# Kernel tuning notes

Hardware: AMD Instinct MI355X
Metric: run time of the kernel (lower is better)

Reference implementation:

```python
import jax, jax.numpy as jnp
import numpy as np

BIAS = 7  # FP8 E4M3 exponent bias


def _decode(bits):
    # bits [..., 8] in order [s, e3, e2, e1, e0, m2, m1, m0]
    b = bits.astype(jnp.int32)
    s = b[..., 0]
    e = (b[..., 1] << 3) | (b[..., 2] << 2) | (b[..., 3] << 1) | b[..., 4]
    m = (b[..., 5] << 2) | (b[..., 6] << 1) | b[..., 7]
    return s, e, m


def _rne_rshift(M, sh):
    # round-to-nearest-even right shift of non-negative int M by sh (sh >= 0)
    q = M >> sh
    rem = M - (q << sh)
    half = jnp.right_shift(jnp.left_shift(1, sh), 1)  # 2^(sh-1), 0 when sh==0
    up = ((rem > half) | ((rem == half) & ((q & 1) == 1))) & (sh > 0)
    return q + up.astype(jnp.int32)


def setup_inputs() -> dict:
    key = jax.random.key(0)
    ks = jax.random.split(key, 6)
    shape = (1024, 4096)

    def make(k1, k2, k3):
        s = jax.random.randint(k1, shape, 0, 2)
        e = jax.random.randint(k2, shape, 0, 15)  # exclude e=15 (NaN region) for well-defined inputs
        m = jax.random.randint(k3, shape, 0, 8)
        bits = jnp.stack([s, (e >> 3) & 1, (e >> 2) & 1, (e >> 1) & 1, e & 1,
                          (m >> 2) & 1, (m >> 1) & 1, m & 1], axis=-1)
        return bits.astype(jnp.float32)

    return {"a": make(ks[0], ks[1], ks[2]), "b": make(ks[3], ks[4], ks[5])}


def _fp8_mul(a, b):
    sa, ea, ma = _decode(a)
    sb, eb_, mb = _decode(b)
    # significand with implicit bit; subnormals (e==0) use leading-zero-normalized form,
    # identical math to the module's mux_a_leading / shift_calc path
    sig_a = jnp.where(ea == 0, ma, ma + 8)
    sig_b = jnp.where(eb_ == 0, mb, mb + 8)
    exa = jnp.where(ea == 0, 1, ea) - BIAS
    exb = jnp.where(eb_ == 0, 1, eb_) - BIAS
    M = sig_a * sig_b              # exact 8-bit product, <= 225 (the 4x4 array multiplier)
    E = exa + exb - 6              # value = M * 2^E  (each sig in units of 2^-3)
    # MSB position p of M (M in [1, 225] => p in [0, 7])
    p = sum(((M >= (1 << k)).astype(jnp.int32) for k in range(1, 8)), start=jnp.zeros_like(M))
    eb_out = E + p + BIAS          # candidate biased exponent (normalization unit)
    # ---- normal path (eb_out >= 1): RNE round to 3 mantissa bits ----
    sh = p - 3
    shp = jnp.maximum(sh, 0)
    lsh = jnp.maximum(-sh, 0)
    mant4 = jnp.left_shift(_rne_rshift(M, shp), lsh)  # in [8, 16]
    carry = mant4 >> 4                                # rounding overflow -> exp += 1
    mant4 = jnp.where(mant4 == 16, 8, mant4)
    e_n = eb_out + carry
    m_n = mant4 - 8
    nan = e_n >= 16                                   # exponent overflow -> NaN (e=1111, m=111)
    e_n = jnp.where(nan, 15, e_n)
    m_n = jnp.where(nan, 7, m_n)
    # ---- subnormal path (eb_out <= 0): mant = RNE(M * 2^(E+9)), value = mant * 2^-9 ----
    t = E + 9
    mant_s = jnp.left_shift(_rne_rshift(M, jnp.clip(-t, 0, 30)), jnp.maximum(t, 0))
    e_s = jnp.where(mant_s >= 8, 1, 0)                # rounding promoted to smallest normal
    m_s = jnp.where(mant_s >= 8, 0, mant_s)
    # ---- select ----
    is_sub = eb_out <= 0
    e_o = jnp.where(is_sub, e_s, e_n)
    m_o = jnp.where(is_sub, m_s, m_n)
    zero = M == 0                                     # either input true zero
    e_o = jnp.where(zero, 0, e_o)
    m_o = jnp.where(zero, 0, m_o)
    s_o = sa ^ sb
    bits = jnp.stack([s_o, (e_o >> 3) & 1, (e_o >> 2) & 1, (e_o >> 1) & 1, e_o & 1,
                      (m_o >> 2) & 1, (m_o >> 1) & 1, m_o & 1], axis=-1)
    return bits.astype(jnp.float32)


def reference(a, b):
    return _fp8_mul(a, b)
```

## Files before the change

kernel.cpp:

```cpp
#include <hip/hip_runtime.h>


#define BIAS 7

__device__ __forceinline__ int rne_rshift(int M, int sh) {
    int q = M >> sh;
    int rem = M - (q << sh);
    int half = (1 << sh) >> 1;
    int up = ((rem > half) | ((rem == half) & (q & 1))) & (sh > 0);
    return q + up;
}

__global__ void __launch_bounds__(256)
fp8_mul_kernel(const float4* __restrict__ a, const float4* __restrict__ b,
               float4* __restrict__ out, int n_groups) {
    int i = blockIdx.x * blockDim.x + threadIdx.x;
    if (i >= n_groups) return;

    float4 a0 = a[2 * i];
    float4 a1 = a[2 * i + 1];
    float4 b0 = b[2 * i];
    float4 b1 = b[2 * i + 1];

    int sa = (int)a0.x;
    int ea = ((int)a0.y << 3) | ((int)a0.z << 2) | ((int)a0.w << 1) | (int)a1.x;
    int ma = ((int)a1.y << 2) | ((int)a1.z << 1) | (int)a1.w;
    int sb = (int)b0.x;
    int eb = ((int)b0.y << 3) | ((int)b0.z << 2) | ((int)b0.w << 1) | (int)b1.x;
    int mb = ((int)b1.y << 2) | ((int)b1.z << 1) | (int)b1.w;

    int sig_a = (ea == 0) ? ma : (ma + 8);
    int sig_b = (eb == 0) ? mb : (mb + 8);
    int exa = ((ea == 0) ? 1 : ea) - BIAS;
    int exb = ((eb == 0) ? 1 : eb) - BIAS;

    int M = sig_a * sig_b;
    int E = exa + exb - 6;

    int p = (M > 0) ? (31 - __clz(M)) : 0;
    int eb_out = E + p + BIAS;

    int sh  = p - 3;
    int shp = (sh > 0) ? sh : 0;
    int lsh = (sh < 0) ? -sh : 0;
    int mant4 = rne_rshift(M, shp) << lsh;
    int carry = mant4 >> 4;
    if (mant4 == 16) mant4 = 8;
    int e_n = eb_out + carry;
    int m_n = mant4 - 8;
    if (e_n >= 16) { e_n = 15; m_n = 7; }

    int t = E + 9;
    int rsh = (-t < 0) ? 0 : ((-t > 30) ? 30 : -t);
    int lsh_s = (t > 0) ? t : 0;
    int mant_s = rne_rshift(M, rsh) << lsh_s;
    int e_s = (mant_s >= 8) ? 1 : 0;
    int m_s = (mant_s >= 8) ? 0 : mant_s;

    int is_sub = (eb_out <= 0);
    int e_o = is_sub ? e_s : e_n;
    int m_o = is_sub ? m_s : m_n;
    if (M == 0) { e_o = 0; m_o = 0; }
    int s_o = sa ^ sb;

    float4 o0, o1;
    o0.x = (float)s_o;
    o0.y = (float)((e_o >> 3) & 1);
    o0.z = (float)((e_o >> 2) & 1);
    o0.w = (float)((e_o >> 1) & 1);
    o1.x = (float)(e_o & 1);
    o1.y = (float)((m_o >> 2) & 1);
    o1.z = (float)((m_o >> 1) & 1);
    o1.w = (float)(m_o & 1);
    out[2 * i]     = o0;
    out[2 * i + 1] = o1;
}

extern "C" void kernel_launch(void* const* d_in, const int* in_sizes, int n_in,
                              void* d_out, int out_size, void* d_ws, size_t ws_size,
                              hipStream_t stream) {
    const float4* a = (const float4*)d_in[0];
    const float4* b = (const float4*)d_in[1];
    float4* out = (float4*)d_out;
    int n_groups = in_sizes[0] / 8;
    int block = 256;
    int grid = (n_groups + block - 1) / block;
    fp8_mul_kernel<<<grid, block, 0, stream>>>(a, b, out, n_groups);
}
```

Measured before the change: 302.6 us.

## Split each FP8 element across two lanes with shuffle exchange and bit-test loads

Each thread now loads one float4 (half of an element's 8 bit-floats) from each input and reads the bits as uint nonzero tests instead of float-to-int conversions. The two lanes of a pair swap nibbles via __shfl_xor, both redundantly compute the FP8 product, and each writes its own half of the output. This doubles thread count and makes every lane access a contiguous 16-byte vector, aiming for better memory coalescing and more loads in flight on a bandwidth-bound kernel. The cost is duplicated arithmetic and a cross-lane shuffle per element.

```diff
diff --git a/kernel.cpp b/kernel.cpp
--- a/kernel.cpp
+++ b/kernel.cpp
@@ -11,23 +11,10 @@
     return q + up;
 }
 
-__global__ void __launch_bounds__(256)
-fp8_mul_kernel(const float4* __restrict__ a, const float4* __restrict__ b,
-               float4* __restrict__ out, int n_groups) {
-    int i = blockIdx.x * blockDim.x + threadIdx.x;
-    if (i >= n_groups) return;
-
-    float4 a0 = a[2 * i];
-    float4 a1 = a[2 * i + 1];
-    float4 b0 = b[2 * i];
-    float4 b1 = b[2 * i + 1];
-
-    int sa = (int)a0.x;
-    int ea = ((int)a0.y << 3) | ((int)a0.z << 2) | ((int)a0.w << 1) | (int)a1.x;
-    int ma = ((int)a1.y << 2) | ((int)a1.z << 1) | (int)a1.w;
-    int sb = (int)b0.x;
-    int eb = ((int)b0.y << 3) | ((int)b0.z << 2) | ((int)b0.w << 1) | (int)b1.x;
-    int mb = ((int)b1.y << 2) | ((int)b1.z << 1) | (int)b1.w;
+__device__ __forceinline__ int fp8_mul_byte(int a8, int b8) {
+    int sa = a8 >> 7,        sb_ = b8 >> 7;
+    int ea = (a8 >> 3) & 15, eb = (b8 >> 3) & 15;
+    int ma = a8 & 7,         mb = b8 & 7;
 
     int sig_a = (ea == 0) ? ma : (ma + 8);
     int sig_b = (eb == 0) ? mb : (mb + 8);
@@ -51,7 +38,7 @@
     if (e_n >= 16) { e_n = 15; m_n = 7; }
 
     int t = E + 9;
-    int rsh = (-t < 0) ? 0 : ((-t > 30) ? 30 : -t);
+    int rsh   = (-t < 0) ? 0 : ((-t > 30) ? 30 : -t);
     int lsh_s = (t > 0) ? t : 0;
     int mant_s = rne_rshift(M, rsh) << lsh_s;
     int e_s = (mant_s >= 8) ? 1 : 0;
@@ -61,29 +48,49 @@
     int e_o = is_sub ? e_s : e_n;
     int m_o = is_sub ? m_s : m_n;
     if (M == 0) { e_o = 0; m_o = 0; }
-    int s_o = sa ^ sb;
+    int s_o = sa ^ sb_;
+    return (s_o << 7) | (e_o << 3) | m_o;
+}
 
-    float4 o0, o1;
-    o0.x = (float)s_o;
-    o0.y = (float)((e_o >> 3) & 1);
-    o0.z = (float)((e_o >> 2) & 1);
-    o0.w = (float)((e_o >> 1) & 1);
-    o1.x = (float)(e_o & 1);
-    o1.y = (float)((m_o >> 2) & 1);
-    o1.z = (float)((m_o >> 1) & 1);
-    o1.w = (float)(m_o & 1);
-    out[2 * i]     = o0;
-    out[2 * i + 1] = o1;
+__global__ void __launch_bounds__(256)
+fp8_mul_kernel(const uint4* __restrict__ a, const uint4* __restrict__ b,
+               float4* __restrict__ out, int n_vec) {
+    int j = blockIdx.x * blockDim.x + threadIdx.x;
+    if (j >= n_vec) return;
+
+    uint4 av = a[j];
+    uint4 bv = b[j];
+
+    int na = ((av.x != 0) << 3) | ((av.y != 0) << 2) | ((av.z != 0) << 1) | (int)(av.w != 0);
+    int nb = ((bv.x != 0) << 3) | ((bv.y != 0) << 2) | ((bv.z != 0) << 1) | (int)(bv.w != 0);
+    int own = na | (nb << 4);
+    int pp  = __shfl_xor(own, 1);
+
+    int odd = j & 1;
+    int a8 = odd ? (((pp  & 0xF) << 4) |  (own & 0xF))
+                 : (((own & 0xF) << 4) |  (pp  & 0xF));
+    int b8 = odd ? ((((pp  >> 4) & 0xF) << 4) | ((own >> 4) & 0xF))
+                 : ((((own >> 4) & 0xF) << 4) | ((pp  >> 4) & 0xF));
+
+    int r = fp8_mul_byte(a8, b8);
+
+    int sbit = odd ? 3 : 7;
+    float4 o;
+    o.x = (float)((r >> sbit)       & 1);
+    o.y = (float)((r >> (sbit - 1)) & 1);
+    o.z = (float)((r >> (sbit - 2)) & 1);
+    o.w = (float)((r >> (sbit - 3)) & 1);
+    out[j] = o;
 }
 
 extern "C" void kernel_launch(void* const* d_in, const int* in_sizes, int n_in,
                               void* d_out, int out_size, void* d_ws, size_t ws_size,
                               hipStream_t stream) {
-    const float4* a = (const float4*)d_in[0];
-    const float4* b = (const float4*)d_in[1];
+    const uint4* a = (const uint4*)d_in[0];
+    const uint4* b = (const uint4*)d_in[1];
     float4* out = (float4*)d_out;
-    int n_groups = in_sizes[0] / 8;
+    int n_vec = in_sizes[0] / 4;
     int block = 256;
-    int grid = (n_groups + block - 1) / block;
-    fp8_mul_kernel<<<grid, block, 0, stream>>>(a, b, out, n_groups);
+    int grid = (n_vec + block - 1) / block;
+    fp8_mul_kernel<<<grid, block, 0, stream>>>(a, b, out, n_vec);
 }
```

New measurement: 299.1 us. About the same (-1.2%).
